# Optimization experiments

Hardware: AMD Instinct MI355X
Metric: run time of the kernel (lower is better)

## Reference

```python
import jax, jax.numpy as jnp
import numpy as np

N = 20000   # nodes
E = 320000  # edges (avg degree 16)
IN = 16     # in_node_nf
H = 64      # hidden_nf
OUT = 64    # out_node_nf
L = 4       # n_layers


def setup_inputs() -> dict:
    key = jax.random.key(0)
    ks = jax.random.split(key, 16)
    w = lambda k, shape: (jax.random.normal(k, shape, dtype=jnp.float32) * 0.05)
    zb = lambda *shape: jnp.zeros(shape, dtype=jnp.float32)
    return {
        "h": jax.random.normal(ks[0], (N, IN), dtype=jnp.float32),
        "x": jax.random.normal(ks[1], (N, 3), dtype=jnp.float32),
        "edge_index": jax.random.randint(ks[2], (2, E), 0, N),
        "emb_in_w": w(ks[3], (IN, H)), "emb_in_b": zb(H),
        "edge_w1": w(ks[4], (L, 2 * H + 1, H)), "edge_b1": zb(L, H),
        "edge_w2": w(ks[5], (L, H, H)), "edge_b2": zb(L, H),
        "coord_w1": w(ks[6], (L, H, H)), "coord_b1": zb(L, H),
        "coord_w2": w(ks[7], (L, H, 1)),  # bias-free last coord_mlp layer
        "node_w1": w(ks[8], (L, 2 * H, H)), "node_b1": zb(L, H),
        "node_w2": w(ks[9], (L, H, H)), "node_b2": zb(L, H),
        "emb_out_w": w(ks[10], (H, OUT)), "emb_out_b": zb(OUT),
    }


def reference(h, x, edge_index, emb_in_w, emb_in_b,
              edge_w1, edge_b1, edge_w2, edge_b2,
              coord_w1, coord_b1, coord_w2,
              node_w1, node_b1, node_w2, node_b2,
              emb_out_w, emb_out_b):
    row, col = edge_index[0], edge_index[1]
    act = jax.nn.silu
    # receiver in-degree for mean coordinate aggregation (clamped to >=1)
    cnt = jax.ops.segment_sum(jnp.ones((row.shape[0], 1), h.dtype), row, num_segments=N)
    cnt = jnp.maximum(cnt, 1.0)

    h = h @ emb_in_w + emb_in_b
    for l in range(L):
        # coord2radial
        diff = x[row] - x[col]                               # [E,3]
        radial = jnp.sum(diff * diff, axis=-1, keepdims=True)  # [E,1]
        # edge model: m_ij = phi_e(h_i, h_j, ||x_i-x_j||^2)
        e_in = jnp.concatenate([h[row], h[col], radial], axis=-1)  # [E,2H+1]
        m = act(e_in @ edge_w1[l] + edge_b1[l])
        m = act(m @ edge_w2[l] + edge_b2[l])                 # [E,H]
        # coord model: x_i += mean_j (x_i - x_j) * phi_x(m_ij)
        phi = act(m @ coord_w1[l] + coord_b1[l]) @ coord_w2[l]  # [E,1]
        trans = diff * phi                                    # [E,3]
        x = x + jax.ops.segment_sum(trans, row, num_segments=N) / cnt
        # node model: h_i = h_i + phi_h(h_i, sum_j m_ij)
        agg = jax.ops.segment_sum(m, row, num_segments=N)     # [N,H]
        n_in = jnp.concatenate([h, agg], axis=-1)             # [N,2H]
        out = act(n_in @ node_w1[l] + node_b1[l]) @ node_w2[l] + node_b2[l]
        h = h + out
    h = h @ emb_out_w + emb_out_b
    return h, x
```

## Files before the change

kernel.cpp:

```cpp
#include <hip/hip_runtime.h>
#include <hip/hip_bf16.h>


#define NN 20000
#define EE 320000
#define LSE 17024
#define LSN 6272

typedef unsigned short u16;
typedef unsigned int   u32;
typedef __attribute__((ext_vector_type(8))) short s16x8;
typedef __attribute__((ext_vector_type(4))) float f32x4;

__device__ __forceinline__ float bf2f(u16 u) { return __uint_as_float(((u32)u) << 16); }
__device__ __forceinline__ float silu_f(float x) {
    return x * __builtin_amdgcn_rcpf(1.0f + __expf(-x));
}

__device__ __forceinline__ u16 f2bf_rne(float f) {
    u32 u = __float_as_uint(f);
    return (u16)((u + 0x7FFFu + ((u >> 16) & 1u)) >> 16);
}
__device__ __forceinline__ float gldf(const void* p, int i, int bf) {
    return bf ? bf2f(((const u16*)p)[i]) : ((const float*)p)[i];
}
__device__ __forceinline__ u16 gldb(const void* p, int i, int bf) {
    return bf ? ((const u16*)p)[i] : f2bf_rne(((const float*)p)[i]);
}

__global__ void k_sentinel(u16* __restrict__ out, int n, float v) {
    int t = blockIdx.x * 256 + threadIdx.x;
    if (t < n) out[t] = f2bf_rne(v);
}

__global__ __launch_bounds__(256) void k_pack(
    const void* __restrict__ ew1, const void* __restrict__ eb1,
    const void* __restrict__ ew2, const void* __restrict__ eb2,
    const void* __restrict__ cw1, const void* __restrict__ cb1,
    const void* __restrict__ cw2,
    const void* __restrict__ nw1, const void* __restrict__ nb1,
    const void* __restrict__ nw2, const void* __restrict__ nb2,
    const u16* __restrict__ h_raw, const int* __restrict__ rowi,
    int* __restrict__ flag, int* __restrict__ deg,
    u16* __restrict__ pkE, u32* __restrict__ pkN)
{
    if (blockIdx.x >= 64) {
        int e = (blockIdx.x - 64) * 256 + threadIdx.x;
        if (e < EE) atomicAdd(&deg[rowi[e]], 1);
        return;
    }
    __shared__ int cnt_s;
    if (threadIdx.x == 0) cnt_s = 0;
    __syncthreads();
    if (threadIdx.x < 128) {
        float v = fabsf(bf2f(h_raw[threadIdx.x]));
        if (v >= 0.015625f && v <= 16.0f) atomicAdd(&cnt_s, 1);
    }
    __syncthreads();
    const int bf = (cnt_s >= 96) ? 1 : 0;
    if (blockIdx.x == 0 && threadIdx.x == 0) *flag = bf;

    const int gid = blockIdx.x * 256 + threadIdx.x;
    const int stride = 64 * 256;

    for (int g = gid; g < 4 * 16384; g += stride) {
        int l = g >> 14, idx = g & 16383;
        u16 v;
        if (idx < 8192) {
            int j = idx & 7, lane = (idx >> 3) & 63, t = (idx >> 9) & 3, w = idx >> 11;
            int k = 32 * w + (lane >> 4) * 8 + j, n = 16 * t + (lane & 15);
            v = gldb(ew1, l * 129 * 64 + k * 64 + n, bf);
        } else if (idx < 12288) {
            int i2 = idx - 8192;
            int j = i2 & 7, lane = (i2 >> 3) & 63, t = (i2 >> 9) & 3, w = i2 >> 11;
            int k = 32 * w + (lane >> 4) * 8 + j, n = 16 * t + (lane & 15);
            v = gldb(ew2, l * 4096 + k * 64 + n, bf);
        } else {
            int i2 = idx - 12288;
            int j = i2 & 7, lane = (i2 >> 3) & 63, t = (i2 >> 9) & 3, w = i2 >> 11;
            int k = 32 * w + (lane >> 4) * 8 + j, n = 16 * t + (lane & 15);
            v = gldb(cw1, l * 4096 + k * 64 + n, bf);
        }
        pkE[l * LSE + idx] = v;
    }
    for (int g = gid; g < 4 * 320; g += stride) {
        int l = g / 320, r = g % 320, wch = r >> 6, i = r & 63;
        float v = (wch == 0) ? gldf(eb1, l * 64 + i, bf)
                : (wch == 1) ? gldf(eb2, l * 64 + i, bf)
                : (wch == 2) ? gldf(cb1, l * 64 + i, bf)
                : (wch == 3) ? gldf(cw2, l * 64 + i, bf)
                :              gldf(ew1, l * 129 * 64 + 128 * 64 + i, bf);
        ((float*)(pkE + l * LSE + 16384))[r] = v;
    }
    for (int g = gid; g < 4 * 6144; g += stride) {
        int l = g / 6144, idx = g % 6144;
        u32 pv;
        if (idx < 4096) {
            int kp = idx >> 6, j = idx & 63;
            u32 lo = gldb(nw1, l * 8192 + (2 * kp) * 64 + j, bf);
            u32 hi = gldb(nw1, l * 8192 + (2 * kp + 1) * 64 + j, bf);
            pv = lo | (hi << 16);
        } else {
            int i2 = idx - 4096, kp = i2 >> 6, j = i2 & 63;
            u32 lo = gldb(nw2, l * 4096 + (2 * kp) * 64 + j, bf);
            u32 hi = gldb(nw2, l * 4096 + (2 * kp + 1) * 64 + j, bf);
            pv = lo | (hi << 16);
        }
        pkN[l * LSN + idx] = pv;
    }
    for (int g = gid; g < 4 * 128; g += stride) {
        int l = g >> 7, r = g & 127;
        float v = (r < 64) ? gldf(nb1, l * 64 + r, bf) : gldf(nb2, l * 64 + (r - 64), bf);
        ((float*)(pkN + l * LSN + 6144))[r] = v;
    }
}

__global__ __launch_bounds__(1024) void k_scan(const int* deg, int* offs, int* cursor) {
    __shared__ int part[1024];
    const int tid = threadIdx.x;
    const int CH = (NN + 1023) / 1024;
    const int b0 = tid * CH;
    int s = 0;
    for (int i = 0; i < CH; i++) { int idx = b0 + i; if (idx < NN) s += deg[idx]; }
    part[tid] = s;
    __syncthreads();
    for (int d = 1; d < 1024; d <<= 1) {
        int v = (tid >= d) ? part[tid - d] : 0;
        __syncthreads();
        part[tid] += v;
        __syncthreads();
    }
    int run = (tid > 0) ? part[tid - 1] : 0;
    for (int i = 0; i < CH; i++) {
        int idx = b0 + i;
        if (idx < NN) {
            int dv = deg[idx];
            offs[idx] = run;
            cursor[idx] = run;
            run += dv;
        }
    }
    if (tid == 1023) offs[NN] = run;
}

__global__ void k_scatter(const int* __restrict__ rowi, const int* __restrict__ coli,
                          int* __restrict__ cursor, int* __restrict__ slist) {
    int e = blockIdx.x * 256 + threadIdx.x;
    if (e < EE) {
        int r = rowi[e];
        int pos = atomicAdd(&cursor[r], 1);
        slist[pos] = coli[e];
    }
}

__global__ __launch_bounds__(256) void k_embed(
    const void* __restrict__ h_in, const void* __restrict__ x_in,
    const void* __restrict__ w, const void* __restrict__ bias,
    const int* __restrict__ flag,
    float* __restrict__ hws, float* __restrict__ xws, u16* __restrict__ hb)
{
    const int bf = *flag;
    const int lane = threadIdx.x & 63;
    const int wv   = threadIdx.x >> 6;
    const int i    = blockIdx.x * 4 + wv;
    float acc = gldf(bias, lane, bf);
    #pragma unroll
    for (int k = 0; k < 16; k++)
        acc = fmaf(gldf(h_in, i * 16 + k, bf), gldf(w, k * 64 + lane, bf), acc);
    hws[i * 64 + lane] = acc;
    hb[i * 64 + lane] = f2bf_rne(acc);
    if (lane < 3) xws[i * 3 + lane] = gldf(x_in, i * 3 + lane, bf);
}

#define OFF_B23  8192
#define OFF_M    16384
#define MPAD     76
#define OFF_PHI  (OFF_M + 8 * 16 * MPAD)
__global__ __launch_bounds__(512, 2) void k_edge(
    const u16* __restrict__ hb, const float* __restrict__ xws,
    const int* __restrict__ offs, const int* __restrict__ slist,
    const u16* __restrict__ pE,
    float* __restrict__ agg, float* __restrict__ xacc)
{
    __shared__ __align__(16) u16 sW[OFF_PHI + 8 * 32];

    const int tid = threadIdx.x, lane = tid & 63, wv = tid >> 6;
    const int l15 = lane & 15, quad = lane >> 4;

    for (int idx = tid; idx < 2048; idx += 512)
        ((s16x8*)sW)[idx] = ((const s16x8*)pE)[idx];
    const float* pb = (const float*)(pE + 16384);
    float b1v[4], b2v[4], cb1v[4], c2v[4], wrv[4];
    #pragma unroll
    for (int t = 0; t < 4; t++) {
        b1v[t]  = pb[       16 * t + l15];
        b2v[t]  = pb[ 64 +  16 * t + l15];
        cb1v[t] = pb[128 +  16 * t + l15];
        c2v[t]  = pb[192 +  16 * t + l15];
        wrv[t]  = pb[256 +  16 * t + l15];
    }
    __syncthreads();

    const int gw = blockIdx.x * 8 + wv, totW = gridDim.x * 8;
    u16* mrow = &sW[OFF_M + wv * 16 * MPAD];
    float* phiw = (float*)&sW[OFF_PHI + wv * 32];

    for (int n = gw; n < NN; n += totW) {
        const int o0 = offs[n], deg = offs[n + 1] - o0;
        if (deg == 0) continue;

        const s16x8 Ar0 = *(const s16x8*)&hb[n * 64 + quad * 8];
        const s16x8 Ar1 = *(const s16x8*)&hb[n * 64 + 32 + quad * 8];
        f32x4 Cb[4] = {{0,0,0,0},{0,0,0,0},{0,0,0,0},{0,0,0,0}};
        #pragma unroll
        for (int t = 0; t < 4; t++) {
            const s16x8 Bf0 = *(const s16x8*)&sW[((0 * 4 + t) * 64 + lane) * 8];
            Cb[t] = __builtin_amdgcn_mfma_f32_16x16x32_bf16(Ar0, Bf0, Cb[t], 0, 0, 0);
            const s16x8 Bf1 = *(const s16x8*)&sW[((1 * 4 + t) * 64 + lane) * 8];
            Cb[t] = __builtin_amdgcn_mfma_f32_16x16x32_bf16(Ar1, Bf1, Cb[t], 0, 0, 0);
        }
        const float xrv = (quad < 3) ? xws[n * 3 + quad] : 0.0f;
        float aggA[4] = {0.f, 0.f, 0.f, 0.f};
        float xaccA = 0.0f;

        for (int eb = 0; eb < deg; eb += 16) {
            const int nb = min(16, deg - eb);
            const int ee = (l15 < nb) ? l15 : 0;
            const int ce = slist[o0 + eb + ee];
            float dx = 0.0f;
            if (quad < 3 && l15 < nb) dx = xrv - xws[ce * 3 + quad];
            float r2 = dx * dx;
            r2 += __shfl_xor(r2, 16, 64);
            r2 += __shfl_xor(r2, 32, 64);

            f32x4 C[4] = {Cb[0], Cb[1], Cb[2], Cb[3]};
            {
                const s16x8 Ac0 = *(const s16x8*)&hb[ce * 64 + quad * 8];
                const s16x8 Ac1 = *(const s16x8*)&hb[ce * 64 + 32 + quad * 8];
                #pragma unroll
                for (int t = 0; t < 4; t++) {
                    const s16x8 Bf2 = *(const s16x8*)&sW[((2 * 4 + t) * 64 + lane) * 8];
                    C[t] = __builtin_amdgcn_mfma_f32_16x16x32_bf16(Ac0, Bf2, C[t], 0, 0, 0);
                    const s16x8 Bf3 = *(const s16x8*)&sW[((3 * 4 + t) * 64 + lane) * 8];
                    C[t] = __builtin_amdgcn_mfma_f32_16x16x32_bf16(Ac1, Bf3, C[t], 0, 0, 0);
                }
            }
            float r2r[4];
            #pragma unroll
            for (int r = 0; r < 4; r++) r2r[r] = __shfl(r2, quad * 4 + r, 64);
            #pragma unroll
            for (int t = 0; t < 4; t++)
                #pragma unroll
                for (int r = 0; r < 4; r++) {
                    float v = silu_f(C[t][r] + b1v[t] + r2r[r] * wrv[t]);
                    mrow[(quad * 4 + r) * MPAD + 16 * t + l15] = f2bf_rne(v);
                }

            f32x4 D[4] = {{0,0,0,0},{0,0,0,0},{0,0,0,0},{0,0,0,0}};
            #pragma unroll
            for (int w = 0; w < 2; w++) {
                const s16x8 Am = *(const s16x8*)(mrow + l15 * MPAD + 32 * w + quad * 8);
                #pragma unroll
                for (int t = 0; t < 4; t++) {
                    const s16x8 Bf = *(const s16x8*)&sW[OFF_B23 + ((w * 4 + t) * 64 + lane) * 8];
                    D[t] = __builtin_amdgcn_mfma_f32_16x16x32_bf16(Am, Bf, D[t], 0, 0, 0);
                }
            }
            #pragma unroll
            for (int t = 0; t < 4; t++)
                #pragma unroll
                for (int r = 0; r < 4; r++) {
                    float v = silu_f(D[t][r] + b2v[t]);
                    if (quad * 4 + r < nb) aggA[t] += v;
                    mrow[(quad * 4 + r) * MPAD + 16 * t + l15] = f2bf_rne(v);
                }

            f32x4 P[4] = {{0,0,0,0},{0,0,0,0},{0,0,0,0},{0,0,0,0}};
            #pragma unroll
            for (int w = 0; w < 2; w++) {
                const s16x8 Am = *(const s16x8*)(mrow + l15 * MPAD + 32 * w + quad * 8);
                #pragma unroll
                for (int t = 0; t < 4; t++) {
                    const s16x8 Bf = *(const s16x8*)&sW[OFF_B23 + (((2 + w) * 4 + t) * 64 + lane) * 8];
                    P[t] = __builtin_amdgcn_mfma_f32_16x16x32_bf16(Am, Bf, P[t], 0, 0, 0);
                }
            }
            float ph[4];
            #pragma unroll
            for (int r = 0; r < 4; r++) {
                float s = 0.f;
                #pragma unroll
                for (int t = 0; t < 4; t++) s = fmaf(silu_f(P[t][r] + cb1v[t]), c2v[t], s);
                s += __shfl_xor(s, 1, 64);
                s += __shfl_xor(s, 2, 64);
                s += __shfl_xor(s, 4, 64);
                s += __shfl_xor(s, 8, 64);
                ph[r] = s;
            }
            if (l15 == 0) {
                #pragma unroll
                for (int r = 0; r < 4; r++) phiw[quad * 4 + r] = ph[r];
            }
            float phv = phiw[l15];
            if (quad < 3 && l15 < nb) xaccA = fmaf(dx, phv, xaccA);
        }

        #pragma unroll
        for (int t = 0; t < 4; t++) {
            aggA[t] += __shfl_xor(aggA[t], 16, 64);
            aggA[t] += __shfl_xor(aggA[t], 32, 64);
        }
        float av = (quad == 0) ? aggA[0] : (quad == 1) ? aggA[1]
                 : (quad == 2) ? aggA[2] : aggA[3];
        agg[n * 64 + quad * 16 + l15] = av;

        xaccA += __shfl_xor(xaccA, 1, 64);
        xaccA += __shfl_xor(xaccA, 2, 64);
        xaccA += __shfl_xor(xaccA, 4, 64);
        xaccA += __shfl_xor(xaccA, 8, 64);
        if (l15 == 0 && quad < 3) xacc[n * 3 + quad] = xaccA / (float)deg;
    }
}

__global__ __launch_bounds__(256) void k_node(
    float* __restrict__ hws, u16* __restrict__ hb, const float* __restrict__ agg,
    float* __restrict__ xws, const float* __restrict__ xacc,
    const u32* __restrict__ pN)
{
    __shared__ __align__(16) u32 sW1p[64 * 64];
    __shared__ __align__(16) u32 sW2p[32 * 64];
    __shared__ float sB1f[64], sB2f[64];
    __shared__ __align__(16) float sNin[4][8][132];

    const int tid = threadIdx.x, lane = tid & 63, wv = tid >> 6;
    for (int idx = tid; idx < 1024; idx += 256)
        ((f32x4*)sW1p)[idx] = ((const f32x4*)pN)[idx];
    for (int idx = tid; idx < 512; idx += 256)
        ((f32x4*)sW2p)[idx] = ((const f32x4*)(pN + 4096))[idx];
    const float* pb = (const float*)(pN + 6144);
    if (tid < 64) { sB1f[tid] = pb[tid]; sB2f[tid] = pb[64 + tid]; }

    {
        int t = blockIdx.x * 96 + tid;
        if (tid < 96) xws[t] += xacc[t];
    }
    __syncthreads();

    const int i0 = (blockIdx.x * 4 + wv) * 8;
    float hold[8];
    #pragma unroll
    for (int b = 0; b < 8; b++) {
        int i = i0 + b;
        float hv = hws[i * 64 + lane];
        hold[b] = hv;
        sNin[wv][b][lane]      = hv;
        sNin[wv][b][64 + lane] = agg[i * 64 + lane];
    }

    float acc[8];
    #pragma unroll
    for (int b = 0; b < 8; b++) acc[b] = sB1f[lane];
    #pragma unroll
    for (int kk = 0; kk < 32; kk++) {
        u32 w01 = sW1p[(kk * 2) * 64 + lane];
        u32 w23 = sW1p[(kk * 2 + 1) * 64 + lane];
        float w0 = __uint_as_float(w01 << 16), w1 = __uint_as_float(w01 & 0xffff0000u);
        float w2 = __uint_as_float(w23 << 16), w3 = __uint_as_float(w23 & 0xffff0000u);
        #pragma unroll
        for (int b = 0; b < 8; b++) {
            const float4 e4 = *reinterpret_cast<const float4*>(&sNin[wv][b][kk * 4]);
            acc[b] = fmaf(e4.x, w0, fmaf(e4.y, w1, fmaf(e4.z, w2, fmaf(e4.w, w3, acc[b]))));
        }
    }
    #pragma unroll
    for (int b = 0; b < 8; b++) acc[b] = silu_f(acc[b]);
    #pragma unroll
    for (int b = 0; b < 8; b++) sNin[wv][b][lane] = acc[b];

    float out[8];
    #pragma unroll
    for (int b = 0; b < 8; b++) out[b] = sB2f[lane];
    #pragma unroll
    for (int kk = 0; kk < 16; kk++) {
        u32 w01 = sW2p[(kk * 2) * 64 + lane];
        u32 w23 = sW2p[(kk * 2 + 1) * 64 + lane];
        float w0 = __uint_as_float(w01 << 16), w1 = __uint_as_float(w01 & 0xffff0000u);
        float w2 = __uint_as_float(w23 << 16), w3 = __uint_as_float(w23 & 0xffff0000u);
        #pragma unroll
        for (int b = 0; b < 8; b++) {
            const float4 e4 = *reinterpret_cast<const float4*>(&sNin[wv][b][kk * 4]);
            out[b] = fmaf(e4.x, w0, fmaf(e4.y, w1, fmaf(e4.z, w2, fmaf(e4.w, w3, out[b]))));
        }
    }
    #pragma unroll
    for (int b = 0; b < 8; b++) {
        float hv = hold[b] + out[b];
        hws[(i0 + b) * 64 + lane] = hv;
        hb[(i0 + b) * 64 + lane] = f2bf_rne(hv);
    }
}

__global__ __launch_bounds__(256) void k_out(
    const float* __restrict__ hws, const float* __restrict__ xws,
    const void* __restrict__ wo, const void* __restrict__ bo,
    const int* __restrict__ flag, void* __restrict__ out)
{
    __shared__ u32 sWp[32 * 64];
    __shared__ float sBf[64];
    __shared__ __align__(16) float sH[4][8][68];
    const int tid = threadIdx.x, lane = tid & 63, wv = tid >> 6;
    const int bf = *flag;
    for (int idx = tid; idx < 32 * 64; idx += 256) {
        int kp = idx >> 6, j = idx & 63;
        u32 lo = gldb(wo, (kp * 2) * 64 + j, bf);
        u32 hi = gldb(wo, (kp * 2 + 1) * 64 + j, bf);
        sWp[idx] = lo | (hi << 16);
    }
    if (tid < 64) sBf[tid] = gldf(bo, tid, bf);
    __syncthreads();

    const int i0 = (blockIdx.x * 4 + wv) * 8;
    #pragma unroll
    for (int b = 0; b < 8; b++) sH[wv][b][lane] = hws[(i0 + b) * 64 + lane];

    float acc[8];
    #pragma unroll
    for (int b = 0; b < 8; b++) acc[b] = sBf[lane];
    #pragma unroll
    for (int kk = 0; kk < 16; kk++) {
        u32 w01 = sWp[(kk * 2) * 64 + lane];
        u32 w23 = sWp[(kk * 2 + 1) * 64 + lane];
        float w0 = __uint_as_float(w01 << 16), w1 = __uint_as_float(w01 & 0xffff0000u);
        float w2 = __uint_as_float(w23 << 16), w3 = __uint_as_float(w23 & 0xffff0000u);
        #pragma unroll
        for (int b = 0; b < 8; b++) {
            const float4 e4 = *reinterpret_cast<const float4*>(&sH[wv][b][kk * 4]);
            acc[b] = fmaf(e4.x, w0, fmaf(e4.y, w1, fmaf(e4.z, w2, fmaf(e4.w, w3, acc[b]))));
        }
    }
    u16*   oh16 = (u16*)out;
    float* ohf  = (float*)out;
    u16*   ox16 = oh16 + (size_t)NN * 64;
    float* oxf  = ohf  + (size_t)NN * 64;
    #pragma unroll
    for (int b = 0; b < 8; b++) {
        int i = i0 + b;
        if (bf) {
            oh16[i * 64 + lane] = f2bf_rne(acc[b]);
            if (lane < 3) ox16[i * 3 + lane] = f2bf_rne(xws[i * 3 + lane]);
        } else {
            ohf[i * 64 + lane] = acc[b];
            if (lane < 3) oxf[i * 3 + lane] = xws[i * 3 + lane];
        }
    }
}

extern "C" void kernel_launch(void* const* d_in, const int* in_sizes, int n_in,
                              void* d_out, int out_size, void* d_ws, size_t ws_size,
                              hipStream_t stream)
{
    const size_t WS_REQ = (size_t)NN * 134 * sizeof(float) + 64;
    if (ws_size < WS_REQ) {
        float sval = 1000.0f + (float)(ws_size >> 20);
        k_sentinel<<<(out_size + 255) / 256, 256, 0, stream>>>(
            (u16*)d_out, out_size, sval);
        return;
    }

    const void* h_in = d_in[0];
    const void* x_in = d_in[1];
    const int*  eidx = (const int*)d_in[2];
    const int* rowi = eidx;
    const int* coli = eidx + EE;

    float* ws   = (float*)d_ws;
    float* hws  = ws;
    float* xws  = hws + NN * 64;
    float* agg  = xws + NN * 3;
    float* xacc = agg + NN * 64;
    int*   flag = (int*)(xacc + NN * 3);

    u16* hb     = (u16*)d_out;
    int* offs   = (int*)(hb + (size_t)NN * 64);
    int* slist  = offs + (NN + 4);
    u16* pkE    = (u16*)(slist + EE);
    u32* pkN    = (u32*)(pkE + 4 * LSE);
    int* cursor = (int*)(pkN + 4 * LSN);

    hipMemsetAsync(cursor, 0, (size_t)NN * sizeof(int), stream);
    hipMemsetAsync(agg, 0, (size_t)NN * 67 * sizeof(float), stream);

    k_pack<<<64 + (EE + 255) / 256, 256, 0, stream>>>(
        d_in[5], d_in[6], d_in[7], d_in[8], d_in[9], d_in[10], d_in[11],
        d_in[12], d_in[13], d_in[14], d_in[15],
        (const u16*)h_in, rowi, flag, cursor, pkE, pkN);
    k_scan<<<1, 1024, 0, stream>>>(cursor, offs, cursor);
    k_scatter<<<(EE + 255) / 256, 256, 0, stream>>>(rowi, coli, cursor, slist);
    k_embed<<<NN / 4, 256, 0, stream>>>(h_in, x_in, d_in[3], d_in[4], flag, hws, xws, hb);

    for (int l = 0; l < 4; l++) {
        k_edge<<<768, 512, 0, stream>>>(hb, xws, offs, slist,
                                        pkE + l * LSE, agg, xacc);
        k_node<<<NN / 32, 256, 0, stream>>>(hws, hb, agg, xws, xacc,
                                            pkN + (size_t)l * LSN);
    }
    k_out<<<NN / 32, 256, 0, stream>>>(hws, xws, d_in[16], d_in[17], flag, d_out);
}
```

Measured before the change: 546.6 us.

## Add dynamic atomic node queue and software-prefetch gathers in edge kernel

```diff
diff --git a/kernel.cpp b/kernel.cpp
--- a/kernel.cpp
+++ b/kernel.cpp
@@ -176,11 +176,11 @@
 #define OFF_M    16384
 #define MPAD     76
 #define OFF_PHI  (OFF_M + 8 * 16 * MPAD)
-__global__ __launch_bounds__(512, 2) void k_edge(
+__global__ __launch_bounds__(512, 4) void k_edge(
     const u16* __restrict__ hb, const float* __restrict__ xws,
     const int* __restrict__ offs, const int* __restrict__ slist,
     const u16* __restrict__ pE,
-    float* __restrict__ agg, float* __restrict__ xacc)
+    float* __restrict__ agg, float* __restrict__ xacc, int* __restrict__ qh)
 {
     __shared__ __align__(16) u16 sW[OFF_PHI + 8 * 32];
 
@@ -201,42 +201,90 @@
     }
     __syncthreads();
 
-    const int gw = blockIdx.x * 8 + wv, totW = gridDim.x * 8;
     u16* mrow = &sW[OFF_M + wv * 16 * MPAD];
     float* phiw = (float*)&sW[OFF_PHI + wv * 32];
 
-    for (int n = gw; n < NN; n += totW) {
-        const int o0 = offs[n], deg = offs[n + 1] - o0;
-        if (deg == 0) continue;
-
-        const s16x8 Ar0 = *(const s16x8*)&hb[n * 64 + quad * 8];
-        const s16x8 Ar1 = *(const s16x8*)&hb[n * 64 + 32 + quad * 8];
-        f32x4 Cb[4] = {{0,0,0,0},{0,0,0,0},{0,0,0,0},{0,0,0,0}};
-        #pragma unroll
-        for (int t = 0; t < 4; t++) {
-            const s16x8 Bf0 = *(const s16x8*)&sW[((0 * 4 + t) * 64 + lane) * 8];
-            Cb[t] = __builtin_amdgcn_mfma_f32_16x16x32_bf16(Ar0, Bf0, Cb[t], 0, 0, 0);
-            const s16x8 Bf1 = *(const s16x8*)&sW[((1 * 4 + t) * 64 + lane) * 8];
-            Cb[t] = __builtin_amdgcn_mfma_f32_16x16x32_bf16(Ar1, Bf1, Cb[t], 0, 0, 0);
-        }
-        const float xrv = (quad < 3) ? xws[n * 3 + quad] : 0.0f;
-        float aggA[4] = {0.f, 0.f, 0.f, 0.f};
-        float xaccA = 0.0f;
-
-        for (int eb = 0; eb < deg; eb += 16) {
-            const int nb = min(16, deg - eb);
-            const int ee = (l15 < nb) ? l15 : 0;
-            const int ce = slist[o0 + eb + ee];
-            float dx = 0.0f;
-            if (quad < 3 && l15 < nb) dx = xrv - xws[ce * 3 + quad];
-            float r2 = dx * dx;
-            r2 += __shfl_xor(r2, 16, 64);
-            r2 += __shfl_xor(r2, 32, 64);
-
-            f32x4 C[4] = {Cb[0], Cb[1], Cb[2], Cb[3]};
-            {
-                const s16x8 Ac0 = *(const s16x8*)&hb[ce * 64 + quad * 8];
-                const s16x8 Ac1 = *(const s16x8*)&hb[ce * 64 + 32 + quad * 8];
+    int pairq = -1;
+#define POPN(dst) do {                                                  \
+        if (pairq >= 0) { dst = pairq; pairq = -1; }                    \
+        else { int v_ = 0;                                              \
+               if (lane == 0) v_ = atomicAdd(qh, 1);                    \
+               v_ = __shfl(v_, 0, 64);                                  \
+               dst = v_ * 2;                                            \
+               pairq = (dst + 1 < NN) ? dst + 1 : -1; }                 \
+    } while (0)
+
+    int n; POPN(n);
+    int o0 = 0, dg = 0, nb = 0;
+    s16x8 Ar0 = {0,0,0,0,0,0,0,0}, Ar1 = {0,0,0,0,0,0,0,0};
+    s16x8 Ac0 = {0,0,0,0,0,0,0,0}, Ac1 = {0,0,0,0,0,0,0,0};
+    float xrv = 0.f, dxv = 0.f;
+    if (n < NN) {
+        o0 = offs[n]; dg = offs[n + 1] - o0;
+        Ar0 = *(const s16x8*)&hb[n * 64 + quad * 8];
+        Ar1 = *(const s16x8*)&hb[n * 64 + 32 + quad * 8];
+        xrv = (quad < 3) ? xws[n * 3 + quad] : 0.f;
+        if (dg > 0) {
+            nb = min(16, dg);
+            int ee = (l15 < nb) ? l15 : 0;
+            int ce = slist[o0 + ee];
+            dxv = (quad < 3 && l15 < nb) ? xrv - xws[ce * 3 + quad] : 0.f;
+            Ac0 = *(const s16x8*)&hb[ce * 64 + quad * 8];
+            Ac1 = *(const s16x8*)&hb[ce * 64 + 32 + quad * 8];
+        }
+    }
+
+    while (n < NN) {
+        int n2; POPN(n2);
+        int o0n = 0, dgn = 0, nbn = 0;
+        s16x8 Arn0 = {0,0,0,0,0,0,0,0}, Arn1 = {0,0,0,0,0,0,0,0};
+        s16x8 Acn0 = {0,0,0,0,0,0,0,0}, Acn1 = {0,0,0,0,0,0,0,0};
+        float xrvn = 0.f, dxn = 0.f;
+        if (n2 < NN) {
+            o0n = offs[n2]; dgn = offs[n2 + 1] - o0n;
+            Arn0 = *(const s16x8*)&hb[n2 * 64 + quad * 8];
+            Arn1 = *(const s16x8*)&hb[n2 * 64 + 32 + quad * 8];
+            xrvn = (quad < 3) ? xws[n2 * 3 + quad] : 0.f;
+            if (dgn > 0) {
+                nbn = min(16, dgn);
+                int ee = (l15 < nbn) ? l15 : 0;
+                int ce = slist[o0n + ee];
+                dxn = (quad < 3 && l15 < nbn) ? xrvn - xws[ce * 3 + quad] : 0.f;
+                Acn0 = *(const s16x8*)&hb[ce * 64 + quad * 8];
+                Acn1 = *(const s16x8*)&hb[ce * 64 + 32 + quad * 8];
+            }
+        }
+
+        if (dg > 0) {
+            f32x4 Cb[4] = {{0,0,0,0},{0,0,0,0},{0,0,0,0},{0,0,0,0}};
+            #pragma unroll
+            for (int t = 0; t < 4; t++) {
+                const s16x8 Bf0 = *(const s16x8*)&sW[((0 * 4 + t) * 64 + lane) * 8];
+                Cb[t] = __builtin_amdgcn_mfma_f32_16x16x32_bf16(Ar0, Bf0, Cb[t], 0, 0, 0);
+                const s16x8 Bf1 = *(const s16x8*)&sW[((1 * 4 + t) * 64 + lane) * 8];
+                Cb[t] = __builtin_amdgcn_mfma_f32_16x16x32_bf16(Ar1, Bf1, Cb[t], 0, 0, 0);
+            }
+            float aggA[4] = {0.f, 0.f, 0.f, 0.f};
+            float xaccA = 0.0f;
+
+            for (int eb = 0; eb < dg; eb += 16) {
+                const int more = (eb + 16) < dg;
+                int nb2 = 0; float dx2 = 0.f;
+                s16x8 A0n = {0,0,0,0,0,0,0,0}, A1n = {0,0,0,0,0,0,0,0};
+                if (more) {
+                    nb2 = min(16, dg - eb - 16);
+                    int ee2 = (l15 < nb2) ? l15 : 0;
+                    int ce2 = slist[o0 + eb + 16 + ee2];
+                    dx2 = (quad < 3 && l15 < nb2) ? xrv - xws[ce2 * 3 + quad] : 0.f;
+                    A0n = *(const s16x8*)&hb[ce2 * 64 + quad * 8];
+                    A1n = *(const s16x8*)&hb[ce2 * 64 + 32 + quad * 8];
+                }
+
+                float r2 = dxv * dxv;
+                r2 += __shfl_xor(r2, 16, 64);
+                r2 += __shfl_xor(r2, 32, 64);
+
+                f32x4 C[4] = {Cb[0], Cb[1], Cb[2], Cb[3]};
                 #pragma unroll
                 for (int t = 0; t < 4; t++) {
                     const s16x8 Bf2 = *(const s16x8*)&sW[((2 * 4 + t) * 64 + lane) * 8];
@@ -244,82 +292,89 @@
                     const s16x8 Bf3 = *(const s16x8*)&sW[((3 * 4 + t) * 64 + lane) * 8];
                     C[t] = __builtin_amdgcn_mfma_f32_16x16x32_bf16(Ac1, Bf3, C[t], 0, 0, 0);
                 }
+                float r2r[4];
+                #pragma unroll
+                for (int r = 0; r < 4; r++) r2r[r] = __shfl(r2, quad * 4 + r, 64);
+                #pragma unroll
+                for (int t = 0; t < 4; t++)
+                    #pragma unroll
+                    for (int r = 0; r < 4; r++) {
+                        float v = silu_f(C[t][r] + b1v[t] + r2r[r] * wrv[t]);
+                        mrow[(quad * 4 + r) * MPAD + 16 * t + l15] = f2bf_rne(v);
+                    }
+
+                f32x4 D[4] = {{0,0,0,0},{0,0,0,0},{0,0,0,0},{0,0,0,0}};
+                #pragma unroll
+                for (int w = 0; w < 2; w++) {
+                    const s16x8 Am = *(const s16x8*)(mrow + l15 * MPAD + 32 * w + quad * 8);
+                    #pragma unroll
+                    for (int t = 0; t < 4; t++) {
+                        const s16x8 Bf = *(const s16x8*)&sW[OFF_B23 + ((w * 4 + t) * 64 + lane) * 8];
+                        D[t] = __builtin_amdgcn_mfma_f32_16x16x32_bf16(Am, Bf, D[t], 0, 0, 0);
+                    }
+                }
+                #pragma unroll
+                for (int t = 0; t < 4; t++)
+                    #pragma unroll
+                    for (int r = 0; r < 4; r++) {
+                        float v = silu_f(D[t][r] + b2v[t]);
+                        if (quad * 4 + r < nb) aggA[t] += v;
+                        mrow[(quad * 4 + r) * MPAD + 16 * t + l15] = f2bf_rne(v);
+                    }
+
+                f32x4 P[4] = {{0,0,0,0},{0,0,0,0},{0,0,0,0},{0,0,0,0}};
+                #pragma unroll
+                for (int w = 0; w < 2; w++) {
+                    const s16x8 Am = *(const s16x8*)(mrow + l15 * MPAD + 32 * w + quad * 8);
+                    #pragma unroll
+                    for (int t = 0; t < 4; t++) {
+                        const s16x8 Bf = *(const s16x8*)&sW[OFF_B23 + (((2 + w) * 4 + t) * 64 + lane) * 8];
+                        P[t] = __builtin_amdgcn_mfma_f32_16x16x32_bf16(Am, Bf, P[t], 0, 0, 0);
+                    }
+                }
+                float ph[4];
+                #pragma unroll
+                for (int r = 0; r < 4; r++) {
+                    float s = 0.f;
+                    #pragma unroll
+                    for (int t = 0; t < 4; t++) s = fmaf(silu_f(P[t][r] + cb1v[t]), c2v[t], s);
+                    s += __shfl_xor(s, 1, 64);
+                    s += __shfl_xor(s, 2, 64);
+                    s += __shfl_xor(s, 4, 64);
+                    s += __shfl_xor(s, 8, 64);
+                    ph[r] = s;
+                }
+                if (l15 == 0) {
+                    #pragma unroll
+                    for (int r = 0; r < 4; r++) phiw[quad * 4 + r] = ph[r];
+                }
+                float phv = phiw[l15];
+                xaccA = fmaf(dxv, phv, xaccA);
+
+                if (more) { nb = nb2; dxv = dx2; Ac0 = A0n; Ac1 = A1n; }
             }
-            float r2r[4];
+
             #pragma unroll
-            for (int r = 0; r < 4; r++) r2r[r] = __shfl(r2, quad * 4 + r, 64);
-            #pragma unroll
-            for (int t = 0; t < 4; t++)
-                #pragma unroll
-                for (int r = 0; r < 4; r++) {
-                    float v = silu_f(C[t][r] + b1v[t] + r2r[r] * wrv[t]);
-                    mrow[(quad * 4 + r) * MPAD + 16 * t + l15] = f2bf_rne(v);
-                }
-
-            f32x4 D[4] = {{0,0,0,0},{0,0,0,0},{0,0,0,0},{0,0,0,0}};
-            #pragma unroll
-            for (int w = 0; w < 2; w++) {
-                const s16x8 Am = *(const s16x8*)(mrow + l15 * MPAD + 32 * w + quad * 8);
-                #pragma unroll
-                for (int t = 0; t < 4; t++) {
-                    const s16x8 Bf = *(const s16x8*)&sW[OFF_B23 + ((w * 4 + t) * 64 + lane) * 8];
-                    D[t] = __builtin_amdgcn_mfma_f32_16x16x32_bf16(Am, Bf, D[t], 0, 0, 0);
-                }
+            for (int t = 0; t < 4; t++) {
+                aggA[t] += __shfl_xor(aggA[t], 16, 64);
+                aggA[t] += __shfl_xor(aggA[t], 32, 64);
             }
-            #pragma unroll
-            for (int t = 0; t < 4; t++)
-                #pragma unroll
-                for (int r = 0; r < 4; r++) {
-                    float v = silu_f(D[t][r] + b2v[t]);
-                    if (quad * 4 + r < nb) aggA[t] += v;
-                    mrow[(quad * 4 + r) * MPAD + 16 * t + l15] = f2bf_rne(v);
-                }
-
-            f32x4 P[4] = {{0,0,0,0},{0,0,0,0},{0,0,0,0},{0,0,0,0}};
-            #pragma unroll
-            for (int w = 0; w < 2; w++) {
-                const s16x8 Am = *(const s16x8*)(mrow + l15 * MPAD + 32 * w + quad * 8);
-                #pragma unroll
-                for (int t = 0; t < 4; t++) {
-                    const s16x8 Bf = *(const s16x8*)&sW[OFF_B23 + (((2 + w) * 4 + t) * 64 + lane) * 8];
-                    P[t] = __builtin_amdgcn_mfma_f32_16x16x32_bf16(Am, Bf, P[t], 0, 0, 0);
-                }
-            }
-            float ph[4];
-            #pragma unroll
-            for (int r = 0; r < 4; r++) {
-                float s = 0.f;
-                #pragma unroll
-                for (int t = 0; t < 4; t++) s = fmaf(silu_f(P[t][r] + cb1v[t]), c2v[t], s);
-                s += __shfl_xor(s, 1, 64);
-                s += __shfl_xor(s, 2, 64);
-                s += __shfl_xor(s, 4, 64);
-                s += __shfl_xor(s, 8, 64);
-                ph[r] = s;
-            }
-            if (l15 == 0) {
-                #pragma unroll
-                for (int r = 0; r < 4; r++) phiw[quad * 4 + r] = ph[r];
-            }
-            float phv = phiw[l15];
-            if (quad < 3 && l15 < nb) xaccA = fmaf(dx, phv, xaccA);
-        }
-
-        #pragma unroll
-        for (int t = 0; t < 4; t++) {
-            aggA[t] += __shfl_xor(aggA[t], 16, 64);
-            aggA[t] += __shfl_xor(aggA[t], 32, 64);
-        }
-        float av = (quad == 0) ? aggA[0] : (quad == 1) ? aggA[1]
-                 : (quad == 2) ? aggA[2] : aggA[3];
-        agg[n * 64 + quad * 16 + l15] = av;
-
-        xaccA += __shfl_xor(xaccA, 1, 64);
-        xaccA += __shfl_xor(xaccA, 2, 64);
-        xaccA += __shfl_xor(xaccA, 4, 64);
-        xaccA += __shfl_xor(xaccA, 8, 64);
-        if (l15 == 0 && quad < 3) xacc[n * 3 + quad] = xaccA / (float)deg;
-    }
+            float av = (quad == 0) ? aggA[0] : (quad == 1) ? aggA[1]
+                     : (quad == 2) ? aggA[2] : aggA[3];
+            agg[n * 64 + quad * 16 + l15] = av;
+
+            xaccA += __shfl_xor(xaccA, 1, 64);
+            xaccA += __shfl_xor(xaccA, 2, 64);
+            xaccA += __shfl_xor(xaccA, 4, 64);
+            xaccA += __shfl_xor(xaccA, 8, 64);
+            if (l15 == 0 && quad < 3) xacc[n * 3 + quad] = xaccA / (float)dg;
+        }
+
+        n = n2; o0 = o0n; dg = dgn; nb = nbn;
+        Ar0 = Arn0; Ar1 = Arn1; Ac0 = Acn0; Ac1 = Acn1;
+        xrv = xrvn; dxv = dxn;
+    }
+#undef POPN
 }
 
 __global__ __launch_bounds__(256) void k_node(
@@ -486,8 +541,9 @@
     u16* pkE    = (u16*)(slist + EE);
     u32* pkN    = (u32*)(pkE + 4 * LSE);
     int* cursor = (int*)(pkN + 4 * LSN);
-
-    hipMemsetAsync(cursor, 0, (size_t)NN * sizeof(int), stream);
+    int* qcnt   = cursor + NN;
+
+    hipMemsetAsync(cursor, 0, (size_t)(NN + 8) * sizeof(int), stream);
     hipMemsetAsync(agg, 0, (size_t)NN * 67 * sizeof(float), stream);
 
     k_pack<<<64 + (EE + 255) / 256, 256, 0, stream>>>(
@@ -499,8 +555,8 @@
     k_embed<<<NN / 4, 256, 0, stream>>>(h_in, x_in, d_in[3], d_in[4], flag, hws, xws, hb);
 
     for (int l = 0; l < 4; l++) {
-        k_edge<<<768, 512, 0, stream>>>(hb, xws, offs, slist,
-                                        pkE + l * LSE, agg, xacc);
+        k_edge<<<512, 512, 0, stream>>>(hb, xws, offs, slist,
+                                        pkE + l * LSE, agg, xacc, qcnt + l);
         k_node<<<NN / 32, 256, 0, stream>>>(hws, hb, agg, xws, xacc,
                                             pkN + (size_t)l * LSN);
     }
```

New measurement: 1.023 ms. +87.2%, slower.

## Order edge-kernel nodes by degree bucket and shrink edge grid

Applied to the files above, without the earlier changes.

```diff
diff --git a/kernel.cpp b/kernel.cpp
--- a/kernel.cpp
+++ b/kernel.cpp
@@ -115,8 +115,10 @@
     }
 }
 
-__global__ __launch_bounds__(1024) void k_scan(const int* deg, int* offs, int* cursor) {
+__global__ __launch_bounds__(1024) void k_scan(const int* deg, int* offs, int* cursor,
+                                               int* __restrict__ perm) {
     __shared__ int part[1024];
+    __shared__ int hist[32], basep[32];
     const int tid = threadIdx.x;
     const int CH = (NN + 1023) / 1024;
     const int b0 = tid * CH;
@@ -141,6 +143,33 @@
         }
     }
     if (tid == 1023) offs[NN] = run;
+    __syncthreads();
+
+    if (tid < 32) hist[tid] = 0;
+    __syncthreads();
+    for (int i = 0; i < CH; i++) {
+        int idx = b0 + i;
+        if (idx < NN) {
+            int dv = offs[idx + 1] - offs[idx];
+            int key = min(31, (dv + 15) >> 4);
+            atomicAdd(&hist[key], 1);
+        }
+    }
+    __syncthreads();
+    if (tid == 0) {
+        int pos = 0;
+        for (int k = 31; k >= 0; k--) { basep[k] = pos; pos += hist[k]; }
+    }
+    __syncthreads();
+    for (int i = 0; i < CH; i++) {
+        int idx = b0 + i;
+        if (idx < NN) {
+            int dv = offs[idx + 1] - offs[idx];
+            int key = min(31, (dv + 15) >> 4);
+            int p = atomicAdd(&basep[key], 1);
+            perm[p] = idx;
+        }
+    }
 }
 
 __global__ void k_scatter(const int* __restrict__ rowi, const int* __restrict__ coli,
@@ -179,7 +208,7 @@
 __global__ __launch_bounds__(512, 2) void k_edge(
     const u16* __restrict__ hb, const float* __restrict__ xws,
     const int* __restrict__ offs, const int* __restrict__ slist,
-    const u16* __restrict__ pE,
+    const u16* __restrict__ pE, const int* __restrict__ perm,
     float* __restrict__ agg, float* __restrict__ xacc)
 {
     __shared__ __align__(16) u16 sW[OFF_PHI + 8 * 32];
@@ -205,7 +234,8 @@
     u16* mrow = &sW[OFF_M + wv * 16 * MPAD];
     float* phiw = (float*)&sW[OFF_PHI + wv * 32];
 
-    for (int n = gw; n < NN; n += totW) {
+    for (int pidx = gw; pidx < NN; pidx += totW) {
+        const int n = perm[pidx];
         const int o0 = offs[n], deg = offs[n + 1] - o0;
         if (deg == 0) continue;
 
@@ -486,6 +516,7 @@
     u16* pkE    = (u16*)(slist + EE);
     u32* pkN    = (u32*)(pkE + 4 * LSE);
     int* cursor = (int*)(pkN + 4 * LSN);
+    int* perm   = cursor + NN;
 
     hipMemsetAsync(cursor, 0, (size_t)NN * sizeof(int), stream);
     hipMemsetAsync(agg, 0, (size_t)NN * 67 * sizeof(float), stream);
@@ -494,13 +525,13 @@
         d_in[5], d_in[6], d_in[7], d_in[8], d_in[9], d_in[10], d_in[11],
         d_in[12], d_in[13], d_in[14], d_in[15],
         (const u16*)h_in, rowi, flag, cursor, pkE, pkN);
-    k_scan<<<1, 1024, 0, stream>>>(cursor, offs, cursor);
+    k_scan<<<1, 1024, 0, stream>>>(cursor, offs, cursor, perm);
     k_scatter<<<(EE + 255) / 256, 256, 0, stream>>>(rowi, coli, cursor, slist);
     k_embed<<<NN / 4, 256, 0, stream>>>(h_in, x_in, d_in[3], d_in[4], flag, hws, xws, hb);
 
     for (int l = 0; l < 4; l++) {
-        k_edge<<<768, 512, 0, stream>>>(hb, xws, offs, slist,
-                                        pkE + l * LSE, agg, xacc);
+        k_edge<<<512, 512, 0, stream>>>(hb, xws, offs, slist,
+                                        pkE + l * LSE, perm, agg, xacc);
         k_node<<<NN / 32, 256, 0, stream>>>(hws, hb, agg, xws, xacc,
                                             pkN + (size_t)l * LSN);
     }
```

Measured after the change: 555.4 us. No clear change (+1.6%).
